# Kernel optimization log

Hardware: AMD Instinct MI355X
Metric: run time of the kernel (lower is better)

The kernel has to match this reference:

```python
import jax, jax.numpy as jnp
import numpy as np

B, N, IN_DIM, OUT = 4, 4096, 3, 40
NPTS = [1024, 256, 64, 16]   # base_points // sampling_ratio
K, FIRST_K = 8, 16
EPS = 1e-5

def gelu(t):
    return jax.nn.gelu(t, approximate=False)  # torch nn.GELU default (erf)

def pdist2(a, b):
    # a: (b,d,m), b: (b,d,n) -> squared pairwise distances (b,m,n)
    aa = jnp.sum(a * a, axis=1)[:, :, None]
    bb = jnp.sum(b * b, axis=1)[:, None, :]
    return aa + bb - 2.0 * jnp.einsum('bdm,bdn->bmn', a, b)

def knn_idx(a, b, k):
    # indices of k nearest points of b for each point of a
    return jax.lax.top_k(-pdist2(a, b), k)[1]

def gather_nbr(x, ind):
    # x: (b,d,n), ind: (b,m,k) -> (b,d,m,k)
    b, d, n = x.shape
    m, k = ind.shape[1], ind.shape[2]
    idx = jnp.broadcast_to(ind.reshape(b, 1, m * k), (b, d, m * k))
    return jnp.take_along_axis(x, idx, axis=2).reshape(b, d, m, k)

def bn(x):
    # BatchNorm (training-mode batch stats, gamma=1, beta=0 as at init)
    ax = (0,) + tuple(range(2, x.ndim))
    mu = jnp.mean(x, axis=ax, keepdims=True)
    var = jnp.mean((x - mu) ** 2, axis=ax, keepdims=True)
    return (x - mu) / jnp.sqrt(var + EPS)

def route(x, nbr):
    # (b,d,n),(b,n,k) -> (b,2d,n,k) : cat([neighbor - center, center])
    sel = gather_nbr(x, nbr)
    xc = x[:, :, :, None]
    return jnp.concatenate([sel - xc, jnp.broadcast_to(xc, sel.shape)], axis=1)

def edge_conv(x, l1, l2, sc, k, nbr=None):
    if nbr is None:
        nbr = knn_idx(x, x, k)  # dynamic graph in feature space
    h = jnp.max(jnp.einsum('of,bfnk->bonk', l1, route(x, nbr)), axis=-1)
    h = gelu(bn(h))
    h = jnp.max(jnp.einsum('of,bfnk->bonk', l2, route(h, nbr)), axis=-1)
    short = x if sc is None else jnp.einsum('of,bfn->bon', sc, x)
    return gelu(bn(short + h))

def fps(xyz, m):
    # farthest point sampling; xyz: (b,3,n) -> indices (b,m); start index 0
    pts = jnp.transpose(xyz, (0, 2, 1))  # (b,n,3)
    b, n, _ = pts.shape
    def body(carry, _):
        dmin, last = carry
        lp = jnp.take_along_axis(pts, last[:, None, None], axis=1)  # (b,1,3)
        d = jnp.sum((pts - lp) ** 2, axis=-1)
        dmin = jnp.minimum(dmin, d)
        nxt = jnp.argmax(dmin, axis=-1).astype(jnp.int32)
        return (dmin, nxt), last
    init = (jnp.full((b, n), jnp.inf, pts.dtype), jnp.zeros((b,), jnp.int32))
    _, inds = jax.lax.scan(body, init, None, length=m)
    return jnp.transpose(inds)  # (b,m)

def _forward(x, xyz, mlp_w, mlp_b, c0_l1, c0_l2, l1s, l2s, scs,
             head_w1, head_w2, head_b2):
    b = x.shape[0]
    nbr0 = knn_idx(xyz, xyz, FIRST_K)
    h = gelu(bn(jnp.einsum('oi,bin->bon', mlp_w, x) + mlp_b[None, :, None]))
    h = edge_conv(h, c0_l1, c0_l2, None, FIRST_K, nbr=nbr0)
    cur = xyz
    for i in range(4):
        m = NPTS[i]
        sind = fps(cur, m)
        sxyz = jnp.take_along_axis(
            cur, jnp.broadcast_to(sind[:, None, :], (b, cur.shape[1], m)), axis=2)
        nbr = knn_idx(sxyz, cur, K)
        cur = jnp.mean(gather_nbr(cur, nbr), axis=-1)      # sampled xyz = nbr mean
        h = jnp.max(gather_nbr(h, nbr), axis=-1)           # sampled feat = nbr max
        h = edge_conv(h, l1s[i], l2s[i], scs[i], K)
    g = jnp.mean(h, axis=-1)                               # global average pool
    g = gelu(bn(g @ head_w1.T))
    return g @ head_w2.T + head_b2[None, :]


def setup_inputs() -> dict:
    key = jax.random.key(0)
    ks = jax.random.split(key, 20)
    def w(k, o, i):
        return (jax.random.normal(k, (o, i), jnp.float32) / np.sqrt(i)).astype(jnp.float32)
    return {
        'x': jax.random.normal(ks[0], (B, IN_DIM, N), jnp.float32),
        'xyz': jax.random.normal(ks[1], (B, 3, N), jnp.float32),
        'mlp_w': w(ks[2], 64, IN_DIM), 'mlp_b': jnp.zeros((64,), jnp.float32),
        'c0_l1': w(ks[3], 64, 128), 'c0_l2': w(ks[4], 64, 128),
        's0_l1': w(ks[5], 64, 128), 's0_l2': w(ks[6], 64, 128),
        's1_l1': w(ks[7], 128, 128), 's1_l2': w(ks[8], 128, 256), 's1_sc': w(ks[9], 128, 64),
        's2_l1': w(ks[10], 256, 256), 's2_l2': w(ks[11], 256, 512), 's2_sc': w(ks[12], 256, 128),
        's3_l1': w(ks[13], 512, 512), 's3_l2': w(ks[14], 512, 1024), 's3_sc': w(ks[15], 512, 256),
        'head_w1': w(ks[16], 256, 512), 'head_w2': w(ks[17], OUT, 256),
        'head_b2': jnp.zeros((OUT,), jnp.float32),
    }


def reference(x, xyz, mlp_w, mlp_b, c0_l1, c0_l2, s0_l1, s0_l2,
              s1_l1, s1_l2, s1_sc, s2_l1, s2_l2, s2_sc, s3_l1, s3_l2, s3_sc,
              head_w1, head_w2, head_b2):
    return _forward(x, xyz, mlp_w, mlp_b, c0_l1, c0_l2,
                    (s0_l1, s1_l1, s2_l1, s3_l1),
                    (s0_l2, s1_l2, s2_l2, s3_l2),
                    (None, s1_sc, s2_sc, s3_sc),
                    head_w1, head_w2, head_b2)
```

## Files before the change

kernel.cpp:

```cpp
#include <hip/hip_runtime.h>
#include <math.h>

#define NCHUNK 32
typedef unsigned long long ull;

__device__ __forceinline__ float gelu_f(float v){
  return 0.5f*v*(1.0f+erff(v*0.70710678118654752440f));
}

__device__ __forceinline__ unsigned flipf(float d){
  unsigned u = __float_as_uint(d);
  return (u & 0x80000000u) ? ~u : (u | 0x80000000u);
}

template<int CTRL>
__device__ __forceinline__ ull dpp64(ull k){
  int lo = __builtin_amdgcn_update_dpp(0, (int)(unsigned)k,       CTRL, 0xF, 0xF, true);
  int hi = __builtin_amdgcn_update_dpp(0, (int)(unsigned)(k>>32), CTRL, 0xF, 0xF, true);
  return ((ull)(unsigned)hi<<32) | (unsigned)lo;
}
__device__ __forceinline__ ull rl64(ull k, int l){
  unsigned lo = (unsigned)__builtin_amdgcn_readlane((int)(unsigned)k, l);
  unsigned hi = (unsigned)__builtin_amdgcn_readlane((int)(unsigned)(k>>32), l);
  return ((ull)hi<<32) | lo;
}
__device__ __forceinline__ ull fmax64(ull a, ull b){
  return (ull)__double_as_longlong(fmax(__longlong_as_double((long long)a),
                                        __longlong_as_double((long long)b)));
}
__device__ __forceinline__ ull wave_fmax(ull k){
  k = fmax64(k, dpp64<0xB1>(k));
  k = fmax64(k, dpp64<0x4E>(k));
  k = fmax64(k, dpp64<0x141>(k));
  k = fmax64(k, dpp64<0x140>(k));
  ull a=rl64(k,0), b=rl64(k,16), c=rl64(k,32), d=rl64(k,48);
  return fmax64(fmax64(a,b), fmax64(c,d));
}
template<int CTRL>
__device__ __forceinline__ double dmin_dpp(double k){
  ull o = dpp64<CTRL>((ull)__double_as_longlong(k));
  return fmin(k, __longlong_as_double((long long)o));
}
__device__ __forceinline__ double wave_dmin(double k){
  k = dmin_dpp<0xB1>(k);
  k = dmin_dpp<0x4E>(k);
  k = dmin_dpp<0x141>(k);
  k = dmin_dpp<0x140>(k);
  ull kb = (ull)__double_as_longlong(k);
  double a = __longlong_as_double((long long)rl64(kb,0));
  double b = __longlong_as_double((long long)rl64(kb,16));
  double c = __longlong_as_double((long long)rl64(kb,32));
  double d = __longlong_as_double((long long)rl64(kb,48));
  return fmin(fmin(a,b), fmin(c,d));
}


template<int K, int T>
__device__ __forceinline__ void knn_body(
    const float* __restrict__ cand, int n,
    const float* __restrict__ qsrc, const int* __restrict__ qidx, int m,
    int* __restrict__ nbr, float* __restrict__ outc,
    int b, int qblk, int qoff, char* smem)
{
  float4* tile = (float4*)smem;
  constexpr int NWV = T/64;
  int wv = threadIdx.x >> 6, lane = threadIdx.x & 63;
  int q = qblk*NWV + wv + qoff;
  const float* cb = cand + (size_t)b*3*n;
  int qi = qidx ? qidx[(size_t)b*m + q] : q;
  const float* qb = qsrc + (size_t)b*3*n;
  float qx = qb[qi], qy = qb[n+qi], qz = qb[2*n+qi];
  float aa = (qx*qx + qy*qy) + qz*qz;

  double a[K];
  #pragma unroll
  for (int k=0;k<K;k++) a[k] = 1e300;

  for (int base=0; base<n; base+=1024){
    int cnt = min(1024, n-base);
    for (int j=threadIdx.x; j<cnt; j+=T){
      float x=cb[base+j], y=cb[n+base+j], z=cb[2*n+base+j];
      tile[j] = make_float4(x,y,z,(x*x+y*y)+z*z);
    }
    __syncthreads();
    int steps = cnt >> 6;
    double jd = (double)(base + lane);
    for (int i=0;i<steps;i++){
      int j = lane + (i<<6);
      float4 c = tile[j];
      float d = aa + c.w - 2.0f*((qx*c.x+qy*c.y)+qz*c.z);
      double key = (double)flipf(d) * 4096.0 + jd;
      if (key < a[K-1]){
        #pragma unroll
        for (int k=K-1;k>=1;k--)
          a[k] = fmin(fmax(a[k-1], key), a[k]);
        a[0] = fmin(a[0], key);
      }
      jd += 64.0;
    }
    __syncthreads();
  }

  double head = a[0];
  int res[K];
  #pragma unroll
  for (int r=0; r<K; r++){
    double mk = wave_dmin(head);
    res[r] = (int)((ull)mk & 4095u);
    if (head == mk){
      #pragma unroll
      for (int i2=0;i2<K-1;i2++) a[i2]=a[i2+1];
      a[K-1] = 1e300;
      head = a[0];
    }
  }
  if (lane == 0){
    int* o = nbr + ((size_t)b*m + q)*K;
    #pragma unroll
    for (int r=0;r<K;r++) o[r] = res[r];
  }
  if (outc != nullptr && lane < 3){
    const float* cd = cb + (size_t)lane*n;
    float s=0;
    #pragma unroll
    for (int k=0;k<K;k++) s += cd[res[k]];
    outc[((size_t)b*3 + lane)*m + q] = s * (1.0f/K);
  }
}

template<int NP, int T, int M>
__device__ __forceinline__ void fps_mw_seg(const float* __restrict__ cur, int n,
                                           int* __restrict__ sind, float* __restrict__ gdmin,
                                           int b, int M0, int M1, char* smem)
{
  constexpr int NW = T/64;
  int tid = threadIdx.x;
  int wv = tid>>6;
  const float* cb = cur + (size_t)b*3*n;
  float4* lp = (float4*)smem;
  ull* wred = (ull*)(smem + sizeof(float4)*NP*T);
  float* gd = gdmin + (size_t)b*n;
  float px[NP], py[NP], pz[NP], dmin[NP];
  unsigned nj[NP];
  #pragma unroll
  for (int s=0;s<NP;s++){
    int j = tid + s*T;
    px[s]=cb[j]; py[s]=cb[n+j]; pz[s]=cb[2*n+j];
    dmin[s] = (M0==0) ? 1e30f : gd[j];
    nj[s] = (unsigned)(~j);
    lp[j] = make_float4(px[s],py[s],pz[s],0.f);
  }
  __syncthreads();
  int ci = (M0==0) ? 0 : sind[(size_t)b*M + (M0-1)];
  float4 w0 = lp[ci];
  float X = w0.x, Y = w0.y, Z = w0.z;
  if (M0==0 && tid==0) sind[(size_t)b*M] = 0;
  __builtin_amdgcn_s_setprio(3);
  int p = 0;
  int s0 = (M0==0) ? 1 : M0;
  for (int step=s0; step<M1; step++){
    ull key[NP];
    #pragma unroll
    for (int s=0;s<NP;s++){
      float dx=px[s]-X, dy=py[s]-Y, dz=pz[s]-Z;
      float d = (dx*dx + dy*dy) + dz*dz;
      float nd = fminf(dmin[s], d);
      dmin[s] = nd;
      key[s] = ((ull)__float_as_uint(nd)<<32) | nj[s];
    }
    #pragma unroll
    for (int w=NP; w>1; w>>=1)
      #pragma unroll
      for (int i=0;i<NP;i++) if (i < (w>>1))
        key[i] = fmax64(key[i], key[i+(w>>1)]);
    ull wk = wave_fmax(key[0]);
    if ((tid&63)==0) wred[p*NW + wv] = wk;
    __syncthreads();
    const ulonglong2* wp2 = (const ulonglong2*)(wred + p*NW);
    ulonglong2 m0 = wp2[0], m1 = wp2[1], m2 = wp2[2], m3 = wp2[3];
    ull gk = fmax64(fmax64(fmax64(m0.x,m0.y), fmax64(m1.x,m1.y)),
                    fmax64(fmax64(m2.x,m2.y), fmax64(m3.x,m3.y)));
    int gi = (int)(~(unsigned)gk);
    if (tid==0) sind[(size_t)b*M + step] = gi;
    float4 wp = lp[gi];
    X=wp.x; Y=wp.y; Z=wp.z;
    p ^= 1;
  }
  __builtin_amdgcn_s_setprio(0);
  #pragma unroll
  for (int s=0;s<NP;s++) gd[tid + s*T] = dmin[s];
}

template<int NP, int M>
__device__ __forceinline__ void fps_sw_body(const float* __restrict__ cur, int n,
                                            int* __restrict__ sind, int b, char* smem)
{
  int lane = threadIdx.x;
  const float* cb = cur + (size_t)b*3*n;
  float4* lp = (float4*)smem;
  float px[NP], py[NP], pz[NP], dmin[NP];
  unsigned nj[NP];
  #pragma unroll
  for (int s=0;s<NP;s++){
    int j = lane + s*64;
    px[s]=cb[j]; py[s]=cb[n+j]; pz[s]=cb[2*n+j]; dmin[s]=1e30f;
    nj[s] = (unsigned)(~j);
    lp[j] = make_float4(px[s],py[s],pz[s],0.f);
  }
  float X = lp[0].x, Y = lp[0].y, Z = lp[0].z;
  if (lane==0) sind[(size_t)b*M] = 0;
  __builtin_amdgcn_s_setprio(3);
  for (int step=1; step<M; step++){
    ull key[NP];
    #pragma unroll
    for (int s=0;s<NP;s++){
      float dx=px[s]-X, dy=py[s]-Y, dz=pz[s]-Z;
      float d = (dx*dx + dy*dy) + dz*dz;
      float nd = fminf(dmin[s], d);
      dmin[s] = nd;
      key[s] = ((ull)__float_as_uint(nd)<<32) | nj[s];
    }
    #pragma unroll
    for (int w=NP; w>1; w>>=1)
      #pragma unroll
      for (int i=0;i<NP;i++) if (i < (w>>1))
        key[i] = fmax64(key[i], key[i+(w>>1)]);
    ull gk = wave_fmax(key[0]);
    int gi = (int)(~(unsigned)gk);
    if (lane==0) sind[(size_t)b*M + step] = gi;
    float4 wp = lp[gi];
    X=wp.x; Y=wp.y; Z=wp.z;
  }
  __builtin_amdgcn_s_setprio(0);
}

template<bool DUAL, bool BN>
__device__ __forceinline__ void gemm_body(
    const float* __restrict__ A, const float* __restrict__ B,
    float* __restrict__ out0, float* __restrict__ out1,
    int M, int N, int Kd, int lda, int ldb, int ldo, int boff,
    long sA, long sB, long sO, const float* __restrict__ part, float invR,
    int bxi, int byi, int bzi, char* smem)
{
  A += (size_t)bzi * sA; B += (size_t)bzi * sB;
  float* o0 = out0 + (size_t)bzi * sO;
  float* o1 = DUAL ? (out1 + (size_t)bzi * sO) : nullptr;
  int rowBase = byi*64, colBase = bxi*64;
  float (*As)[64]  = (float(*)[64])smem;
  float (*Bs0)[64] = (float(*)[64])(smem + 4096);
  float (*Bs1)[64] = (float(*)[64])(smem + 8192);
  float* mu_s = (float*)(smem + 12288);
  float* var_s = mu_s + 512;
  int tid = threadIdx.x;
  if (BN){
    for (int oo=tid; oo<Kd; oo+=blockDim.x){
      float s=0, q=0;
      #pragma unroll 4
      for (int c=0;c<NCHUNK;c++){
        s += part[(size_t)c*1024 + oo];
        q += part[(size_t)(NCHUNK+c)*1024 + oo];
      }
      float mu = s*invR;
      mu_s[oo] = mu;
      var_s[oo] = q*invR - mu*mu;
    }
    __syncthreads();
  }
  int ty = tid>>4, tx = tid&15;
  float acc0[4][4] = {}, acc1[4][4] = {};
  int lr = tid>>2, lk = (tid&3)*4;
  for (int k0=0; k0<Kd; k0+=16) {
    float4 va = make_float4(0,0,0,0);
    int r = rowBase + lr;
    if (r < M) va = *(const float4*)(A + (size_t)r*lda + k0 + lk);
    if (BN){
      int c = k0 + lk;
      va.x = gelu_f((va.x - mu_s[c+0]) / sqrtf(var_s[c+0] + 1e-5f));
      va.y = gelu_f((va.y - mu_s[c+1]) / sqrtf(var_s[c+1] + 1e-5f));
      va.z = gelu_f((va.z - mu_s[c+2]) / sqrtf(var_s[c+2] + 1e-5f));
      va.w = gelu_f((va.w - mu_s[c+3]) / sqrtf(var_s[c+3] + 1e-5f));
    }
    As[lk+0][lr]=va.x; As[lk+1][lr]=va.y; As[lk+2][lr]=va.z; As[lk+3][lr]=va.w;
    float4 vb = make_float4(0,0,0,0), vb2 = make_float4(0,0,0,0);
    int c2 = colBase + lr;
    if (c2 < N) {
      vb = *(const float4*)(B + (size_t)c2*ldb + k0 + lk);
      if (DUAL) vb2 = *(const float4*)(B + (size_t)c2*ldb + boff + k0 + lk);
    }
    Bs0[lk+0][lr]=vb.x; Bs0[lk+1][lr]=vb.y; Bs0[lk+2][lr]=vb.z; Bs0[lk+3][lr]=vb.w;
    if (DUAL) {
      Bs1[lk+0][lr]=vb2.x-vb.x; Bs1[lk+1][lr]=vb2.y-vb.y;
      Bs1[lk+2][lr]=vb2.z-vb.z; Bs1[lk+3][lr]=vb2.w-vb.w;
    }
    __syncthreads();
    #pragma unroll
    for (int kk=0;kk<16;kk++){
      float4 a  = *(const float4*)&As[kk][ty*4];
      float4 b0 = *(const float4*)&Bs0[kk][tx*4];
      float av[4]={a.x,a.y,a.z,a.w};
      float b0v[4]={b0.x,b0.y,b0.z,b0.w};
      #pragma unroll
      for (int i=0;i<4;i++)
        #pragma unroll
        for (int j=0;j<4;j++) acc0[i][j] = fmaf(av[i], b0v[j], acc0[i][j]);
      if (DUAL) {
        float4 b1 = *(const float4*)&Bs1[kk][tx*4];
        float b1v[4]={b1.x,b1.y,b1.z,b1.w};
        #pragma unroll
        for (int i=0;i<4;i++)
          #pragma unroll
          for (int j=0;j<4;j++) acc1[i][j] = fmaf(av[i], b1v[j], acc1[i][j]);
      }
    }
    __syncthreads();
  }
  #pragma unroll
  for (int i=0;i<4;i++){
    int r = rowBase + ty*4 + i;
    if (r < M) {
      #pragma unroll
      for (int j=0;j<4;j++){
        int c = colBase + tx*4 + j;
        if (c < N) {
          o0[(size_t)r*ldo + c] = acc0[i][j];
          if (DUAL) o1[(size_t)r*ldo + c] = acc1[i][j];
        }
      }
    }
  }
}

template<bool DUAL, bool BN>
__device__ __forceinline__ void gemm_body_g(
    const float* __restrict__ A, const float* __restrict__ B,
    float* __restrict__ out0, float* __restrict__ out1,
    int M, int N, int Kd, int lda, int ldb, int ldo, int boff,
    const float* __restrict__ part, float invR,
    int bxi, int byi, char* smem)
{
  int rowBase = byi*64, colBase = bxi*64;
  float (*As)[64]  = (float(*)[64])smem;
  float (*Bs0)[64] = (float(*)[64])(smem + 4096);
  float (*Bs1)[64] = (float(*)[64])(smem + 8192);
  float* mu_s = (float*)(smem + 12288);
  float* var_s = mu_s + 512;
  int tid = threadIdx.x;
  bool act = tid < 256;
  if (BN){
    for (int oo=tid; oo<Kd; oo+=blockDim.x){
      float s=0, q=0;
      #pragma unroll 4
      for (int c=0;c<NCHUNK;c++){
        s += part[(size_t)c*1024 + oo];
        q += part[(size_t)(NCHUNK+c)*1024 + oo];
      }
      float mu = s*invR;
      mu_s[oo] = mu;
      var_s[oo] = q*invR - mu*mu;
    }
    __syncthreads();
  }
  int ty = tid>>4, tx = tid&15;
  float acc0[4][4] = {}, acc1[4][4] = {};
  int lr = tid>>2, lk = (tid&3)*4;
  for (int k0=0; k0<Kd; k0+=16) {
    if (act){
      float4 va = make_float4(0,0,0,0);
      int r = rowBase + lr;
      if (r < M) va = *(const float4*)(A + (size_t)r*lda + k0 + lk);
      if (BN){
        int c = k0 + lk;
        va.x = gelu_f((va.x - mu_s[c+0]) / sqrtf(var_s[c+0] + 1e-5f));
        va.y = gelu_f((va.y - mu_s[c+1]) / sqrtf(var_s[c+1] + 1e-5f));
        va.z = gelu_f((va.z - mu_s[c+2]) / sqrtf(var_s[c+2] + 1e-5f));
        va.w = gelu_f((va.w - mu_s[c+3]) / sqrtf(var_s[c+3] + 1e-5f));
      }
      As[lk+0][lr]=va.x; As[lk+1][lr]=va.y; As[lk+2][lr]=va.z; As[lk+3][lr]=va.w;
      float4 vb = make_float4(0,0,0,0), vb2 = make_float4(0,0,0,0);
      int c2 = colBase + lr;
      if (c2 < N) {
        vb = *(const float4*)(B + (size_t)c2*ldb + k0 + lk);
        if (DUAL) vb2 = *(const float4*)(B + (size_t)c2*ldb + boff + k0 + lk);
      }
      Bs0[lk+0][lr]=vb.x; Bs0[lk+1][lr]=vb.y; Bs0[lk+2][lr]=vb.z; Bs0[lk+3][lr]=vb.w;
      if (DUAL) {
        Bs1[lk+0][lr]=vb2.x-vb.x; Bs1[lk+1][lr]=vb2.y-vb.y;
        Bs1[lk+2][lr]=vb2.z-vb.z; Bs1[lk+3][lr]=vb2.w-vb.w;
      }
    }
    __syncthreads();
    if (act){
      #pragma unroll
      for (int kk=0;kk<16;kk++){
        float4 a  = *(const float4*)&As[kk][ty*4];
        float4 b0 = *(const float4*)&Bs0[kk][tx*4];
        float av[4]={a.x,a.y,a.z,a.w};
        float b0v[4]={b0.x,b0.y,b0.z,b0.w};
        #pragma unroll
        for (int i=0;i<4;i++)
          #pragma unroll
          for (int j=0;j<4;j++) acc0[i][j] = fmaf(av[i], b0v[j], acc0[i][j]);
        if (DUAL) {
          float4 b1 = *(const float4*)&Bs1[kk][tx*4];
          float b1v[4]={b1.x,b1.y,b1.z,b1.w};
          #pragma unroll
          for (int i=0;i<4;i++)
            #pragma unroll
            for (int j=0;j<4;j++) acc1[i][j] = fmaf(av[i], b1v[j], acc1[i][j]);
        }
      }
    }
    __syncthreads();
  }
  if (act){
    #pragma unroll
    for (int i=0;i<4;i++){
      int r = rowBase + ty*4 + i;
      if (r < M) {
        #pragma unroll
        for (int j=0;j<4;j++){
          int c = colBase + tx*4 + j;
          if (c < N) {
            out0[(size_t)r*ldo + c] = acc0[i][j];
            if (DUAL) out1[(size_t)r*ldo + c] = acc1[i][j];
          }
        }
      }
    }
  }
}

__device__ __forceinline__ void gather_elem(
    const float* __restrict__ P, const int* __restrict__ nbr,
    const float* __restrict__ addA, const float* __restrict__ addB,
    float* __restrict__ out, int n_out, int n_src, int O, int K, int total, int e)
{
  if (e >= total) return;
  int o = e % O; int r = e / O;
  int b = r / n_out; int i = r % n_out;
  const int* nb = nbr + ((size_t)b*n_out + i)*K;
  float mx = -1e38f;
  for (int k=0;k<K;k++){
    int j = nb[k];
    float v = P[((size_t)b*n_src + j)*O + o];
    mx = fmaxf(mx, v);
  }
  float res = mx;
  if (addA) res += addA[e];
  if (addB) res = addB[e] + res;
  out[e] = res;
}

__device__ __forceinline__ void gatherbn_body(
    const float* __restrict__ P, const int* __restrict__ nbr,
    const float* __restrict__ part, float invR,
    float* __restrict__ out, float* __restrict__ aa,
    int n_out, int n_src, int O, int K, int blk, char* smem)
{
  float* mu_s = (float*)smem; float* var_s = mu_s + 256; float* sv = var_s + 256;
  int tid = threadIdx.x;
  for (int oo=tid; oo<O; oo+=256){
    float s=0, q=0;
    #pragma unroll 4
    for (int c=0;c<NCHUNK;c++){
      s += part[(size_t)c*1024 + oo];
      q += part[(size_t)(NCHUNK+c)*1024 + oo];
    }
    float mu = s*invR;
    mu_s[oo] = mu;
    var_s[oo] = q*invR - mu*mu;
  }
  __syncthreads();
  int e = blk*256 + tid;
  int o = e % O; int r = e / O;
  int b = r / n_out; int i = r % n_out;
  const int* nb = nbr + ((size_t)b*n_out + i)*K;
  float mu = mu_s[o], sd = sqrtf(var_s[o] + 1e-5f);
  float mx = -1e38f;
  for (int k=0;k<K;k++){
    int j = nb[k];
    float p = P[((size_t)b*n_src + j)*O + o];
    float v = gelu_f((p - mu)/sd);
    mx = fmaxf(mx, v);
  }
  out[e] = mx;
  sv[tid] = mx*mx;
  __syncthreads();
  for (int st=O>>1; st>0; st>>=1){
    if (o < st) sv[tid] += sv[tid+st];
    __syncthreads();
  }
  if (o == 0) aa[r] = sv[tid];
}


#define FPS_SMEM 65664

__global__ __launch_bounds__(512,2) void mega1(
    const float* __restrict__ xyz, const float* __restrict__ x,
    const float* __restrict__ mlpw, const float* __restrict__ mlpb,
    int* __restrict__ sind0, float* __restrict__ gdmin,
    int* __restrict__ nbr0, float* __restrict__ hA, int M0, int M1)
{
  __shared__ __align__(16) char SMEM[FPS_SMEM];
  int bid = blockIdx.x;
  if (bid < 4){
    fps_mw_seg<8,512,1024>(xyz, 4096, sind0, gdmin, bid, M0, M1, SMEM);
  } else if (bid < 4+2048){
    int kb = bid - 4;
    knn_body<16,512>(xyz, 4096, xyz, nullptr, 4096, nbr0, nullptr, kb>>9, kb&511, 0, SMEM);
  } else {
    int e = (bid - 2052)*512 + threadIdx.x;
    if (e < 4*4096*64){
      int o = e & 63; int r = e >> 6;
      int b = r / 4096; int i = r % 4096;
      const float* xb = x + (size_t)b*3*4096;
      hA[e] = ((mlpw[o*3+0]*xb[i] + mlpw[o*3+1]*xb[4096+i]) + mlpw[o*3+2]*xb[2*4096+i]) + mlpb[o];
    }
  }
}

__global__ __launch_bounds__(512,2) void fps_bngelu(
    const float* fcur, int* sind, float* gdmin, int M0, int M1,
    float* __restrict__ xx, const float* __restrict__ part, float invR, int O, int total)
{
  __shared__ __align__(16) char SMEM[FPS_SMEM];
  if (blockIdx.x < 4){
    fps_mw_seg<8,512,1024>(fcur, 4096, sind, gdmin, blockIdx.x, M0, M1, SMEM);
    return;
  }
  float* mu_s = (float*)SMEM; float* var_s = mu_s + 512;
  for (int oo=threadIdx.x; oo<O; oo+=512){
    float s=0, q=0;
    #pragma unroll 4
    for (int c=0;c<NCHUNK;c++){
      s += part[(size_t)c*1024 + oo];
      q += part[(size_t)(NCHUNK+c)*1024 + oo];
    }
    float mu = s*invR;
    mu_s[oo] = mu;
    var_s[oo] = q*invR - mu*mu;
  }
  __syncthreads();
  int e = (blockIdx.x-4)*512 + threadIdx.x;
  if (e >= total) return;
  int o = e % O;
  float v = (xx[e]-mu_s[o]) / sqrtf(var_s[o] + 1e-5f);
  xx[e] = gelu_f(v);
}

template<bool DUAL, bool BN>
__global__ __launch_bounds__(512,2) void fps0_gemm(
    const float* fcur, int* sind, float* gdmin, int M0, int M1,
    const float* A, const float* B, float* out0, float* out1,
    int Mg, int Ng, int Kd, int lda, int ldb, int ldo, int boff,
    const float* part, float invR, int nbx)
{
  __shared__ __align__(16) char SMEM[FPS_SMEM];
  if (blockIdx.x < 4){
    fps_mw_seg<8,512,1024>(fcur, 4096, sind, gdmin, blockIdx.x, M0, M1, SMEM);
    return;
  }
  int l = blockIdx.x - 4;
  gemm_body_g<DUAL,BN>(A,B,out0,out1,Mg,Ng,Kd,lda,ldb,ldo,boff,part,invR, l%nbx, l/nbx, SMEM);
}

__global__ __launch_bounds__(512,2) void fps0_gather_knn(
    const float* fcur, int* sind, float* gdmin, int M0, int M1,
    const float* cand, int n, const float* qsrc, const int* qidx, int m,
    int* nbrOut, float* outc, int KNB,
    const float* P, const int* nbr, const float* addA, const float* addB,
    float* out, int n_out, int n_src, int O, int K, int total)
{
  __shared__ __align__(16) char SMEM[FPS_SMEM];
  if (blockIdx.x < 4){
    fps_mw_seg<8,512,1024>(fcur, 4096, sind, gdmin, blockIdx.x, M0, M1, SMEM);
    return;
  }
  int l = blockIdx.x - 4;
  if (l < KNB){
    knn_body<8,512>(cand, n, qsrc, qidx, m, nbrOut, outc, l>>6, l&63, 0, SMEM);
    return;
  }
  int e = (l-KNB)*512 + threadIdx.x;
  gather_elem(P, nbr, addA, addB, out, n_out, n_src, O, K, total, e);
}

__global__ __launch_bounds__(512,2) void fps0_gather(
    const float* fcur, int* sind, float* gdmin, int M0, int M1,
    const float* P, const int* nbr, const float* addA, const float* addB,
    float* out, int n_out, int n_src, int O, int K, int total)
{
  __shared__ __align__(16) char SMEM[FPS_SMEM];
  if (blockIdx.x < 4){
    fps_mw_seg<8,512,1024>(fcur, 4096, sind, gdmin, blockIdx.x, M0, M1, SMEM);
    return;
  }
  int e = (blockIdx.x-4)*512 + threadIdx.x;
  gather_elem(P, nbr, addA, addB, out, n_out, n_src, O, K, total, e);
}

__global__ __launch_bounds__(512,2) void fps0_stats(
    const float* fcur, int* sind, float* gdmin, int M0, int M1,
    const float* __restrict__ x, int R, int O, float* __restrict__ part)
{
  __shared__ __align__(16) char SMEM[FPS_SMEM];
  if (blockIdx.x < 4){
    fps_mw_seg<8,512,1024>(fcur, 4096, sind, gdmin, blockIdx.x, M0, M1, SMEM);
    return;
  }
  int o = threadIdx.x;
  if (o >= O) return;
  int chunk = blockIdx.x - 4;
  int per = (R + NCHUNK - 1)/NCHUNK;
  int r0 = chunk*per, r1 = min(r0+per, R);
  float s=0, q=0;
  for (int r=r0; r<r1; r++){ float v = x[(size_t)r*O + o]; s+=v; q+=v*v; }
  part[(size_t)chunk*1024 + o] = s;
  part[(size_t)(NCHUNK+chunk)*1024 + o] = q;
}

__global__ __launch_bounds__(256) void knn_wave8(
    const float* cand, int n, const float* qsrc, const int* qidx, int m, int qoff,
    int* nbr, float* outc)
{
  __shared__ __align__(16) char SMEM[16384];
  knn_body<8,256>(cand, n, qsrc, qidx, m, nbr, outc, blockIdx.y, blockIdx.x, qoff, SMEM);
}

template<int NP, int M>
__global__ __launch_bounds__(256) void fps_gatherbn(
    const float* fcur, int fn, int* sind,
    const float* P, const int* nbr, const float* part, float invR,
    float* out, float* aa, int n_out, int n_src, int O, int K)
{
  __shared__ __align__(16) char SMEM[(NP*64*16 > 16384) ? NP*64*16 : 16384];
  if (blockIdx.x < 4){
    if (threadIdx.x < 64) fps_sw_body<NP,M>(fcur, fn, sind, blockIdx.x, SMEM);
    return;
  }
  gatherbn_body(P, nbr, part, invR, out, aa, n_out, n_src, O, K, blockIdx.x-4, SMEM);
}

template<int NP, int M, bool DUAL, bool BN>
__global__ __launch_bounds__(256) void fps_gemm(
    const float* fcur, int fn, int* sind,
    const float* A, const float* B, float* out0, float* out1,
    int Mg, int Ng, int Kd, int lda, int ldb, int ldo, int boff,
    const float* part, float invR, int nbx, int nby)
{
  __shared__ __align__(16) char SMEM[(NP*64*16 > 16896) ? NP*64*16 : 16896];
  if (blockIdx.x < 4){
    if (threadIdx.x < 64) fps_sw_body<NP,M>(fcur, fn, sind, blockIdx.x, SMEM);
    return;
  }
  int l = blockIdx.x - 4;
  int bx = l % nbx, by = (l/nbx) % nby, bz = l/(nbx*nby);
  gemm_body<DUAL,BN>(A,B,out0,out1,Mg,Ng,Kd,lda,ldb,ldo,boff,0,0,0,part,invR,bx,by,bz,SMEM);
}

__global__ __launch_bounds__(256) void knn_gather(
    const float* cand, int n, const float* qsrc, const int* qidx, int m,
    int* nbrOut, float* outc, int KNB,
    const float* P, const int* nbr, const float* addA, const float* addB,
    float* out, int n_out, int n_src, int O, int K, int total)
{
  __shared__ __align__(16) char SMEM[16384];
  if (blockIdx.x < KNB){
    int qpb = m/4;
    knn_body<8,256>(cand, n, qsrc, qidx, m, nbrOut, outc, blockIdx.x/qpb, blockIdx.x%qpb, 0, SMEM);
    return;
  }
  gather_elem(P, nbr, addA, addB, out, n_out, n_src, O, K, total, (blockIdx.x-KNB)*256 + threadIdx.x);
}

__global__ __launch_bounds__(256) void knn_gemm(
    const float* cand, int n, const float* qsrc, const int* qidx, int m,
    int* nbrOut, float* outc, int KNB,
    const float* A, const float* B, float* out0,
    int Mg, int Ng, int Kd, int lda, int ldb, int ldo,
    long sA, long sB, long sO, int nbx, int nby)
{
  __shared__ __align__(16) char SMEM[16896];
  if (blockIdx.x < KNB){
    int qpb = m/4;
    knn_body<8,256>(cand, n, qsrc, qidx, m, nbrOut, outc, blockIdx.x/qpb, blockIdx.x%qpb, 0, SMEM);
    return;
  }
  int l = blockIdx.x - KNB;
  int bx = l % nbx, by = (l/nbx) % nby, bz = l/(nbx*nby);
  gemm_body<false,false>(A,B,out0,nullptr,Mg,Ng,Kd,lda,ldb,ldo,0,sA,sB,sO,nullptr,0.f,bx,by,bz,SMEM);
}

__global__ __launch_bounds__(256) void gram_gemm(
    const float* Ag, float* outg, int Mg, int Kg, long sAg, long sOg,
    int ngx, int ngy, int NG,
    const float* A2, const float* B2, float* o20, float* o21,
    int M2, int N2, int K2, int boff2, int nb2x)
{
  __shared__ __align__(16) char SMEM[16896];
  int l = blockIdx.x;
  if (l < NG){
    int bx = l % ngx, by = (l/ngx) % ngy, bz = l/(ngx*ngy);
    gemm_body<false,false>(Ag,Ag,outg,nullptr,Mg,Mg,Kg,Kg,Kg,Mg,0,sAg,sAg,sOg,nullptr,0.f,bx,by,bz,SMEM);
    return;
  }
  l -= NG;
  gemm_body<true,false>(A2,B2,o20,o21,M2,N2,K2,K2,2*K2,N2,boff2,0,0,0,nullptr,0.f, l%nb2x, l/nb2x, 0, SMEM);
}

template<bool DUAL, bool BN>
__global__ __launch_bounds__(256) void gemm_nt(
    const float* A, const float* B, float* out0, float* out1,
    int M, int N, int Kd, int lda, int ldb, int ldo, int boff,
    long sA, long sB, long sO, const float* part, float invR)
{
  __shared__ __align__(16) char SMEM[16896];
  gemm_body<DUAL,BN>(A,B,out0,out1,M,N,Kd,lda,ldb,ldo,boff,sA,sB,sO,part,invR,
                     blockIdx.x, blockIdx.y, blockIdx.z, SMEM);
}

__global__ __launch_bounds__(256) void gemm2sc(
    const float* A2, const float* B2, float* o20, float* o21, int R, int O2, int O1v,
    const float* part, float invR,
    const float* Asc, const float* Bsc, float* osc, int Cin,
    int nbx, int nby)
{
  __shared__ __align__(16) char SMEM[16896];
  int l = blockIdx.x;
  int half = nbx*nby;
  if (l < half){
    gemm_body<true,true>(A2,B2,o20,o21,R,O2,O1v,O1v,2*O1v,O2,O1v,0,0,0,part,invR, l%nbx, l/nbx, 0, SMEM);
  } else {
    l -= half;
    gemm_body<false,false>(Asc,Bsc,osc,nullptr,R,O2,Cin,Cin,Cin,O2,0,0,0,0,nullptr,0.f, l%nbx, l/nbx, 0, SMEM);
  }
}

__global__ __launch_bounds__(256) void gathermax_kernel(
    const float* P, const int* nbr, const float* addA, const float* addB,
    float* out, int n_out, int n_src, int O, int K, int total)
{
  gather_elem(P, nbr, addA, addB, out, n_out, n_src, O, K, total, blockIdx.x*256 + threadIdx.x);
}

__global__ __launch_bounds__(256) void gatherbn_kernel(
    const float* P, const int* nbr, const float* part, float invR,
    float* out, float* aa, int n_out, int n_src, int O, int K)
{
  __shared__ __align__(16) char SMEM[3072];
  gatherbn_body(P, nbr, part, invR, out, aa, n_out, n_src, O, K, blockIdx.x, SMEM);
}

template<int K>
__global__ __launch_bounds__(256) void topk_wave(
    const float* __restrict__ G, const float* __restrict__ aa, int m,
    int* __restrict__ nbr)
{
  __shared__ float abs_s[1024];
  int b = blockIdx.y;
  int wv = threadIdx.x >> 6, lane = threadIdx.x & 63;
  int q = blockIdx.x*4 + wv;
  const float* ab = aa + (size_t)b*m;
  for (int j=threadIdx.x; j<m; j+=256) abs_s[j] = ab[j];
  __syncthreads();
  float aq = ab[q];
  const float* Gq = G + ((size_t)b*m + q)*m;

  double a[K];
  #pragma unroll
  for (int k=0;k<K;k++) a[k] = 1e300;

  int steps = (m+63)>>6;
  double jd = (double)lane;
  for (int i=0;i<steps;i++){
    int j = lane + (i<<6);
    double key = 1e300;
    if (j < m){
      float g = Gq[j];
      float d = aq + abs_s[j] - 2.0f*g;
      key = (double)flipf(d) * 4096.0 + jd;
    }
    if (key < a[K-1]){
      #pragma unroll
      for (int k=K-1;k>=1;k--)
        a[k] = fmin(fmax(a[k-1], key), a[k]);
      a[0] = fmin(a[0], key);
    }
    jd += 64.0;
  }
  double head = a[0];
  int res[K];
  #pragma unroll
  for (int r=0; r<K; r++){
    double mk = wave_dmin(head);
    res[r] = (int)((ull)mk & 4095u);
    if (head == mk){
      #pragma unroll
      for (int i2=0;i2<K-1;i2++) a[i2]=a[i2+1];
      a[K-1] = 1e300;
      head = a[0];
    }
  }
  if (lane == 0){
    int* o = nbr + ((size_t)b*m + q)*K;
    #pragma unroll
    for (int r=0;r<K;r++) o[r] = res[r];
  }
}

__global__ void stats_part_kernel(const float* __restrict__ x, int R, int O,
                                  float* __restrict__ part)
{
  int o = threadIdx.x;
  int chunk = blockIdx.x;
  int per = (R + NCHUNK - 1)/NCHUNK;
  int r0 = chunk*per, r1 = min(r0+per, R);
  float s=0, q=0;
  for (int r=r0; r<r1; r++){ float v = x[(size_t)r*O + o]; s+=v; q+=v*v; }
  part[(size_t)chunk*1024 + o] = s;
  part[(size_t)(NCHUNK+chunk)*1024 + o] = q;
}

__global__ __launch_bounds__(1024) void head_kernel(const float* __restrict__ h,
    const float* __restrict__ part, float invR,
    const float* __restrict__ w1, const float* __restrict__ w2,
    const float* __restrict__ b2, float* __restrict__ out)
{
  __shared__ __align__(16) float mu_s[512], var_s[512];
  __shared__ __align__(16) float g[4*512];
  __shared__ __align__(16) float t[4*256];
  int tid = threadIdx.x;
  for (int oo=tid; oo<512; oo+=1024){
    float s=0, q=0;
    #pragma unroll 4
    for (int c=0;c<NCHUNK;c++){
      s += part[(size_t)c*1024 + oo];
      q += part[(size_t)(NCHUNK+c)*1024 + oo];
    }
    float mu = s*invR;
    mu_s[oo] = mu;
    var_s[oo] = q*invR - mu*mu;
  }
  __syncthreads();
  for (int e=tid; e<2048; e+=1024){
    int b=e>>9, c=e&511;
    float mu = mu_s[c], sd = sqrtf(var_s[c] + 1e-5f);
    float s=0;
    for (int p=0;p<16;p++){
      float v = h[((size_t)(b*16+p))*512 + c];
      s += gelu_f((v-mu)/sd);
    }
    g[e] = s * (1.0f/16.0f);
  }
  __syncthreads();
  {
    int b = tid>>8, j = tid&255;
    const float4* gr = (const float4*)(g + b*512);
    const float4* wr = (const float4*)(w1 + (size_t)j*512);
    float s=0;
    for (int c=0;c<128;c++){
      float4 a=gr[c], w=wr[c];
      s = fmaf(a.x,w.x, fmaf(a.y,w.y, fmaf(a.z,w.z, fmaf(a.w,w.w, s))));
    }
    t[tid] = s;
  }
  __syncthreads();
  if (tid < 256){
    float v0=t[tid], v1=t[256+tid], v2=t[512+tid], v3=t[768+tid];
    float mu = ((v0+v1)+v2+v3)*0.25f;
    float d0=v0-mu, d1=v1-mu, d2=v2-mu, d3=v3-mu;
    float var = ((d0*d0+d1*d1)+d2*d2+d3*d3)*0.25f;
    float sq = sqrtf(var + 1e-5f);
    t[tid]     = gelu_f(d0/sq);
    t[256+tid] = gelu_f(d1/sq);
    t[512+tid] = gelu_f(d2/sq);
    t[768+tid] = gelu_f(d3/sq);
  }
  __syncthreads();
  if (tid < 160){
    int b = tid/40, o = tid%40;
    const float* tr = t + b*256; const float* wr = w2 + (size_t)o*256;
    float s=0;
    for (int j=0;j<256;j++) s = fmaf(tr[j], wr[j], s);
    out[tid] = s + b2[o];
  }
}

extern "C" void kernel_launch(void* const* d_in, const int* in_sizes, int n_in,
                              void* d_out, int out_size, void* d_ws, size_t ws_size,
                              hipStream_t stream)
{
  const float* x    = (const float*)d_in[0];
  const float* xyz  = (const float*)d_in[1];
  const float* mlpw = (const float*)d_in[2];
  const float* mlpb = (const float*)d_in[3];
  const float* c0l1 = (const float*)d_in[4];
  const float* c0l2 = (const float*)d_in[5];
  const float* L1[4] = {(const float*)d_in[6], (const float*)d_in[8],
                        (const float*)d_in[11], (const float*)d_in[14]};
  const float* L2[4] = {(const float*)d_in[7], (const float*)d_in[9],
                        (const float*)d_in[12], (const float*)d_in[15]};
  const float* SC[4] = {nullptr, (const float*)d_in[10],
                        (const float*)d_in[13], (const float*)d_in[16]};
  const float* hw1 = (const float*)d_in[17];
  const float* hw2 = (const float*)d_in[18];
  const float* hb2 = (const float*)d_in[19];
  float* out = (float*)d_out;

  float* ws = (float*)d_ws;
  const size_t MF = 1024*1024;
  float* D    = ws;
  float* hA   = ws + 4*MF;
  float* hX   = ws + 5*MF;
  float* hP   = ws + 6*MF;
  float* hCT  = ws + 7*MF;
  float* hSH  = ws + 8*MF;
  float* hH1  = ws + 9*MF;
  float* hOUT = ws + 10*MF;
  float* aux  = ws + 11*MF;
  int*   nbr0  = (int*)aux;                 aux += 262144;
  int*   nbrS0 = (int*)aux;                 aux += 32768;
  int*   nbrS1 = (int*)aux;                 aux += 8192;
  int*   nbrS2 = (int*)aux;                 aux += 2048;
  int*   nbrS3 = (int*)aux;                 aux += 512;
  int*   nbrF  = (int*)aux;                 aux += 32768;
  int*   sind0 = (int*)aux;                 aux += 4096;
  int*   sind1 = (int*)aux;                 aux += 1024;
  int*   sind2 = (int*)aux;                 aux += 256;
  int*   sind3 = (int*)aux;                 aux += 64;
  float* aa    = aux;                       aux += 4096;
  float* cur1  = aux;                       aux += 12288;
  float* cur2  = aux;                       aux += 3072;
  float* cur3  = aux;                       aux += 768;
  float* part  = aux;                       aux += 65536;
  float* gdmin = aux;                       aux += 16384;

  int tot0 = 4*4096*64;

  mega1<<<4100, 512, 0, stream>>>(xyz, x, mlpw, mlpb, sind0, gdmin, nbr0, hA, 0, 260);
  stats_part_kernel<<<NCHUNK, 64, 0, stream>>>(hA, 16384, 64, part);
  fps_bngelu<<<4+2048, 512, 0, stream>>>(xyz, sind0, gdmin, 260, 390, hA, part, 1.0f/16384.0f, 64, tot0);
  fps0_gemm<true,false><<<4+256, 512, 0, stream>>>(xyz, sind0, gdmin, 390, 517,
      hA, c0l1, hP, hCT, 16384, 64, 64, 64, 128, 64, 64, nullptr, 0.f, 1);
  fps0_gather_knn<<<4+256+2048, 512, 0, stream>>>(xyz, sind0, gdmin, 517, 644,
      xyz, 4096, xyz, sind0, 1024, nbrS0, cur1, 256,
      hP, nbr0, hCT, nullptr, hH1, 4096, 4096, 64, 16, 1048576);
  stats_part_kernel<<<NCHUNK, 64, 0, stream>>>(hH1, 16384, 64, part);
  fps0_gemm<true,true><<<4+256, 512, 0, stream>>>(xyz, sind0, gdmin, 644, 771,
      hH1, c0l2, hP, hCT, 16384, 64, 64, 64, 128, 64, 64, part, 1.0f/16384.0f, 1);
  fps0_gather<<<4+2048, 512, 0, stream>>>(xyz, sind0, gdmin, 771, 898,
      hP, nbr0, hCT, hA, hOUT, 4096, 4096, 64, 16, 1048576);
  fps0_stats<<<4+NCHUNK, 512, 0, stream>>>(xyz, sind0, gdmin, 898, 1024,
      hOUT, 16384, 64, part);

  knn_wave8<<<dim3(128,4),256,0,stream>>>(xyz, 4096, xyz, sind0, 1024, 512, nbrS0, cur1);

  fps_gatherbn<16,256><<<4+1024,256,0,stream>>>(cur1, 1024, sind1,
      hOUT, nbrS0, part, 1.0f/16384.0f, hX, aa, 1024, 4096, 64, 8);
  knn_gemm<<<256+1024,256,0,stream>>>(cur1, 1024, cur1, sind1, 256, nbrS1, cur2, 256,
      hX, hX, D, 1024, 1024, 64, 64, 64, 1024,
      (long)1024*64, (long)1024*64, (long)1024*1024, 16, 16);
  topk_wave<8><<<dim3(256,4),256,0,stream>>>(D, aa, 1024, nbrF);
  fps_gemm<4,64,true,false><<<4+64,256,0,stream>>>(cur2, 256, sind2,
      hX, L1[0], hP, hCT, 4096, 64, 64, 64, 128, 64, 64, nullptr, 0.f, 1, 64);
  knn_gather<<<64+1024,256,0,stream>>>(cur2, 256, cur2, sind2, 64, nbrS2, cur3, 64,
      hP, nbrF, hCT, nullptr, hH1, 1024, 1024, 64, 8, 262144);
  stats_part_kernel<<<NCHUNK, 64, 0, stream>>>(hH1, 4096, 64, part);
  fps_gemm<1,16,true,true><<<4+64,256,0,stream>>>(cur3, 64, sind3,
      hH1, L2[0], hP, hCT, 4096, 64, 64, 64, 128, 64, 64, part, 1.0f/4096.0f, 1, 64);
  knn_gather<<<16+1024,256,0,stream>>>(cur3, 64, cur3, sind3, 16, nbrS3, nullptr, 16,
      hP, nbrF, hCT, hX, hA, 1024, 1024, 64, 8, 262144);
  stats_part_kernel<<<NCHUNK, 64, 0, stream>>>(hA, 4096, 64, part);

  const int   mArr[3]   = {256, 64, 16};
  const int   nsrcArr[3]= {1024, 256, 64};
  const int   CinArr[3] = {64, 128, 256};
  const int   OArr[3]   = {128, 256, 512};
  const int*  nbrSs[3]  = {nbrS1, nbrS2, nbrS3};
  float* hcur = hA;
  float invRprev = 1.0f/4096.0f;
  for (int s=0;s<3;s++){
    int m = mArr[s], nsrc = nsrcArr[s], Cin = CinArr[s], O1 = OArr[s], O2 = OArr[s];
    int R = 4*m;
    int th = R*Cin;
    gatherbn_kernel<<<th/256,256,0,stream>>>(hcur, nbrSs[s], part, invRprev,
                                             hX, aa, m, nsrc, Cin, 8);
    int ngx = (m+63)/64, ngy = (m+63)/64;
    int NG = ngx*ngy*4;
    int nb1x = (O1+63)/64, nb1y = (R+63)/64;
    gram_gemm<<<NG + nb1x*nb1y, 256, 0, stream>>>(
        hX, D, m, Cin, (long)m*Cin, (long)m*m, ngx, ngy, NG,
        hX, L1[s+1], hP, hCT, R, O1, Cin, Cin, nb1x);
    topk_wave<8><<<dim3(m/4,4),256,0,stream>>>(D, aa, m, nbrF);
    int t1 = R*O1;
    gathermax_kernel<<<(t1+255)/256,256,0,stream>>>(hP, nbrF, hCT, nullptr, hH1, m, m, O1, 8, t1);
    stats_part_kernel<<<NCHUNK, O1, 0, stream>>>(hH1, R, O1, part);
    int nbx = (O2+63)/64, nby = (R+63)/64;
    gemm2sc<<<2*nbx*nby,256,0,stream>>>(hH1, L2[s+1], hP, hCT, R, O2, O1, part, 1.0f/R,
                                        hX, SC[s+1], hSH, Cin, nbx, nby);
    int t2 = R*O2;
    float* outbuf = (s&1) ? hA : hOUT;
    gathermax_kernel<<<(t2+255)/256,256,0,stream>>>(hP, nbrF, hCT, hSH, outbuf, m, m, O2, 8, t2);
    stats_part_kernel<<<NCHUNK, O2, 0, stream>>>(outbuf, R, O2, part);
    hcur = outbuf;
    invRprev = 1.0f/R;
  }

  head_kernel<<<1,1024,0,stream>>>(hcur, part, 1.0f/64.0f, hw1, hw2, hb2, out);
}
```

Before: 1.558 ms.

## Split stage-1 FPS across three kernels and re-pair side tasks to overlap serial work

The 256-step FPS over 1024 points now runs in three resumable segments, carrying min-distances through a global buffer. Each segment rides alongside the gatherbn, gram GEMM and top-k kernels. The later FPS and KNN launches are re-paired with different GEMM and gather work, and the first loop iteration's gatherbn is folded into a KNN launch. The aim is to hide the serial, single-wave FPS chains behind parallel work and cut launches, at the cost of extra global save/restore traffic and more complex dependencies between kernels.

```diff
diff --git a/kernel.cpp b/kernel.cpp
--- a/kernel.cpp
+++ b/kernel.cpp
@@ -125,6 +125,62 @@
     #pragma unroll
     for (int k=0;k<K;k++) s += cd[res[k]];
     outc[((size_t)b*3 + lane)*m + q] = s * (1.0f/K);
+  }
+}
+
+template<int K>
+__device__ __forceinline__ void topk_body(
+    const float* __restrict__ G, const float* __restrict__ aa, int m,
+    int* __restrict__ nbr, int b, int qblk, char* smem)
+{
+  float* abs_s = (float*)smem;
+  int wv = threadIdx.x >> 6, lane = threadIdx.x & 63;
+  int q = qblk*4 + wv;
+  const float* ab = aa + (size_t)b*m;
+  for (int j=threadIdx.x; j<m; j+=256) abs_s[j] = ab[j];
+  __syncthreads();
+  float aq = ab[q];
+  const float* Gq = G + ((size_t)b*m + q)*m;
+
+  double a[K];
+  #pragma unroll
+  for (int k=0;k<K;k++) a[k] = 1e300;
+
+  int steps = (m+63)>>6;
+  double jd = (double)lane;
+  for (int i=0;i<steps;i++){
+    int j = lane + (i<<6);
+    double key = 1e300;
+    if (j < m){
+      float g = Gq[j];
+      float d = aq + abs_s[j] - 2.0f*g;
+      key = (double)flipf(d) * 4096.0 + jd;
+    }
+    if (key < a[K-1]){
+      #pragma unroll
+      for (int k=K-1;k>=1;k--)
+        a[k] = fmin(fmax(a[k-1], key), a[k]);
+      a[0] = fmin(a[0], key);
+    }
+    jd += 64.0;
+  }
+  double head = a[0];
+  int res[K];
+  #pragma unroll
+  for (int r=0; r<K; r++){
+    double mk = wave_dmin(head);
+    res[r] = (int)((ull)mk & 4095u);
+    if (head == mk){
+      #pragma unroll
+      for (int i2=0;i2<K-1;i2++) a[i2]=a[i2+1];
+      a[K-1] = 1e300;
+      head = a[0];
+    }
+  }
+  if (lane == 0){
+    int* o = nbr + ((size_t)b*m + q)*K;
+    #pragma unroll
+    for (int r=0;r<K;r++) o[r] = res[r];
   }
 }
 
@@ -232,6 +288,57 @@
     X=wp.x; Y=wp.y; Z=wp.z;
   }
   __builtin_amdgcn_s_setprio(0);
+}
+
+template<int NP, int M>
+__device__ __forceinline__ void fps_sw_seg(const float* __restrict__ cur, int n,
+                                           int* __restrict__ sind, float* __restrict__ gdmin,
+                                           int b, int M0, int M1, char* smem)
+{
+  int lane = threadIdx.x;
+  const float* cb = cur + (size_t)b*3*n;
+  float4* lp = (float4*)smem;
+  float* gd = gdmin + (size_t)b*n;
+  float px[NP], py[NP], pz[NP], dmin[NP];
+  unsigned nj[NP];
+  #pragma unroll
+  for (int s=0;s<NP;s++){
+    int j = lane + s*64;
+    px[s]=cb[j]; py[s]=cb[n+j]; pz[s]=cb[2*n+j];
+    dmin[s] = (M0==0) ? 1e30f : gd[j];
+    nj[s] = (unsigned)(~j);
+    lp[j] = make_float4(px[s],py[s],pz[s],0.f);
+  }
+  int ci = (M0==0) ? 0 : sind[(size_t)b*M + (M0-1)];
+  float4 w0 = lp[ci];
+  float X = w0.x, Y = w0.y, Z = w0.z;
+  if (M0==0 && lane==0) sind[(size_t)b*M] = 0;
+  __builtin_amdgcn_s_setprio(3);
+  int s0 = (M0==0) ? 1 : M0;
+  for (int step=s0; step<M1; step++){
+    ull key[NP];
+    #pragma unroll
+    for (int s=0;s<NP;s++){
+      float dx=px[s]-X, dy=py[s]-Y, dz=pz[s]-Z;
+      float d = (dx*dx + dy*dy) + dz*dz;
+      float nd = fminf(dmin[s], d);
+      dmin[s] = nd;
+      key[s] = ((ull)__float_as_uint(nd)<<32) | nj[s];
+    }
+    #pragma unroll
+    for (int w=NP; w>1; w>>=1)
+      #pragma unroll
+      for (int i=0;i<NP;i++) if (i < (w>>1))
+        key[i] = fmax64(key[i], key[i+(w>>1)]);
+    ull gk = wave_fmax(key[0]);
+    int gi = (int)(~(unsigned)gk);
+    if (lane==0) sind[(size_t)b*M + step] = gi;
+    float4 wp = lp[gi];
+    X=wp.x; Y=wp.y; Z=wp.z;
+  }
+  __builtin_amdgcn_s_setprio(0);
+  #pragma unroll
+  for (int s=0;s<NP;s++) gd[lane + s*64] = dmin[s];
 }
 
 template<bool DUAL, bool BN>
@@ -628,58 +735,68 @@
   knn_body<8,256>(cand, n, qsrc, qidx, m, nbr, outc, blockIdx.y, blockIdx.x, qoff, SMEM);
 }
 
-template<int NP, int M>
-__global__ __launch_bounds__(256) void fps_gatherbn(
-    const float* fcur, int fn, int* sind,
+__global__ __launch_bounds__(256) void fps1_gatherbn(
+    const float* fcur, int* sind, float* gdmin, int M0, int M1,
     const float* P, const int* nbr, const float* part, float invR,
     float* out, float* aa, int n_out, int n_src, int O, int K)
 {
-  __shared__ __align__(16) char SMEM[(NP*64*16 > 16384) ? NP*64*16 : 16384];
+  __shared__ __align__(16) char SMEM[16384];
+  if (blockIdx.x < 4){
+    if (threadIdx.x < 64) fps_sw_seg<16,256>(fcur, 1024, sind, gdmin, blockIdx.x, M0, M1, SMEM);
+    return;
+  }
+  gatherbn_body(P, nbr, part, invR, out, aa, n_out, n_src, O, K, blockIdx.x-4, SMEM);
+}
+
+__global__ __launch_bounds__(256) void fps1_gram(
+    const float* fcur, int* sind, float* gdmin, int M0, int M1,
+    const float* Ag, float* outg, int Mg, int Kg, long sAg, long sOg, int ngx, int ngy)
+{
+  __shared__ __align__(16) char SMEM[16896];
+  if (blockIdx.x < 4){
+    if (threadIdx.x < 64) fps_sw_seg<16,256>(fcur, 1024, sind, gdmin, blockIdx.x, M0, M1, SMEM);
+    return;
+  }
+  int l = blockIdx.x - 4;
+  int bx = l % ngx, by = (l/ngx) % ngy, bz = l/(ngx*ngy);
+  gemm_body<false,false>(Ag,Ag,outg,nullptr,Mg,Mg,Kg,Kg,Kg,Mg,0,sAg,sAg,sOg,nullptr,0.f,bx,by,bz,SMEM);
+}
+
+__global__ __launch_bounds__(256) void fps1_topk(
+    const float* fcur, int* sind, float* gdmin, int M0, int M1,
+    const float* G, const float* aa, int m, int* nbr)
+{
+  __shared__ __align__(16) char SMEM[16384];
+  if (blockIdx.x < 4){
+    if (threadIdx.x < 64) fps_sw_seg<16,256>(fcur, 1024, sind, gdmin, blockIdx.x, M0, M1, SMEM);
+    return;
+  }
+  int l = blockIdx.x - 4;
+  int qpb = m/4;
+  topk_body<8>(G, aa, m, nbr, l/qpb, l%qpb, SMEM);
+}
+
+template<int NP, int M>
+__global__ __launch_bounds__(256) void fps_gather(
+    const float* fcur, int fn, int* sind,
+    const float* P, const int* nbr, const float* addA, const float* addB,
+    float* out, int n_out, int n_src, int O, int K, int total)
+{
+  __shared__ __align__(16) char SMEM[(NP*64*16 > 4096) ? NP*64*16 : 4096];
   if (blockIdx.x < 4){
     if (threadIdx.x < 64) fps_sw_body<NP,M>(fcur, fn, sind, blockIdx.x, SMEM);
     return;
   }
-  gatherbn_body(P, nbr, part, invR, out, aa, n_out, n_src, O, K, blockIdx.x-4, SMEM);
-}
-
-template<int NP, int M, bool DUAL, bool BN>
-__global__ __launch_bounds__(256) void fps_gemm(
-    const float* fcur, int fn, int* sind,
-    const float* A, const float* B, float* out0, float* out1,
-    int Mg, int Ng, int Kd, int lda, int ldb, int ldo, int boff,
-    const float* part, float invR, int nbx, int nby)
-{
-  __shared__ __align__(16) char SMEM[(NP*64*16 > 16896) ? NP*64*16 : 16896];
-  if (blockIdx.x < 4){
-    if (threadIdx.x < 64) fps_sw_body<NP,M>(fcur, fn, sind, blockIdx.x, SMEM);
-    return;
-  }
-  int l = blockIdx.x - 4;
-  int bx = l % nbx, by = (l/nbx) % nby, bz = l/(nbx*nby);
-  gemm_body<DUAL,BN>(A,B,out0,out1,Mg,Ng,Kd,lda,ldb,ldo,boff,0,0,0,part,invR,bx,by,bz,SMEM);
-}
-
-__global__ __launch_bounds__(256) void knn_gather(
+  gather_elem(P, nbr, addA, addB, out, n_out, n_src, O, K, total, (blockIdx.x-4)*256 + threadIdx.x);
+}
+
+template<bool DUAL, bool BN>
+__global__ __launch_bounds__(256) void knn_gemm2(
     const float* cand, int n, const float* qsrc, const int* qidx, int m,
     int* nbrOut, float* outc, int KNB,
-    const float* P, const int* nbr, const float* addA, const float* addB,
-    float* out, int n_out, int n_src, int O, int K, int total)
-{
-  __shared__ __align__(16) char SMEM[16384];
-  if (blockIdx.x < KNB){
-    int qpb = m/4;
-    knn_body<8,256>(cand, n, qsrc, qidx, m, nbrOut, outc, blockIdx.x/qpb, blockIdx.x%qpb, 0, SMEM);
-    return;
-  }
-  gather_elem(P, nbr, addA, addB, out, n_out, n_src, O, K, total, (blockIdx.x-KNB)*256 + threadIdx.x);
-}
-
-__global__ __launch_bounds__(256) void knn_gemm(
-    const float* cand, int n, const float* qsrc, const int* qidx, int m,
-    int* nbrOut, float* outc, int KNB,
-    const float* A, const float* B, float* out0,
-    int Mg, int Ng, int Kd, int lda, int ldb, int ldo,
-    long sA, long sB, long sO, int nbx, int nby)
+    const float* A, const float* B, float* out0, float* out1,
+    int Mg, int Ng, int Kd, int boff,
+    const float* part, float invR, int nbx)
 {
   __shared__ __align__(16) char SMEM[16896];
   if (blockIdx.x < KNB){
@@ -688,8 +805,22 @@
     return;
   }
   int l = blockIdx.x - KNB;
-  int bx = l % nbx, by = (l/nbx) % nby, bz = l/(nbx*nby);
-  gemm_body<false,false>(A,B,out0,nullptr,Mg,Ng,Kd,lda,ldb,ldo,0,sA,sB,sO,nullptr,0.f,bx,by,bz,SMEM);
+  gemm_body<DUAL,BN>(A,B,out0,out1,Mg,Ng,Kd,Kd,DUAL?2*Kd:Kd,Ng,boff,0,0,0,part,invR, l%nbx, l/nbx, 0, SMEM);
+}
+
+__global__ __launch_bounds__(256) void knn_gatherbn(
+    const float* cand, int n, const float* qsrc, const int* qidx, int m,
+    int* nbrOut, int KNB,
+    const float* P, const int* nbr, const float* part, float invR,
+    float* out, float* aa, int n_out, int n_src, int O, int K)
+{
+  __shared__ __align__(16) char SMEM[16384];
+  if (blockIdx.x < KNB){
+    int qpb = m/4;
+    knn_body<8,256>(cand, n, qsrc, qidx, m, nbrOut, nullptr, blockIdx.x/qpb, blockIdx.x%qpb, 0, SMEM);
+    return;
+  }
+  gatherbn_body(P, nbr, part, invR, out, aa, n_out, n_src, O, K, blockIdx.x-KNB, SMEM);
 }
 
 __global__ __launch_bounds__(256) void gram_gemm(
@@ -707,17 +838,6 @@
   }
   l -= NG;
   gemm_body<true,false>(A2,B2,o20,o21,M2,N2,K2,K2,2*K2,N2,boff2,0,0,0,nullptr,0.f, l%nb2x, l/nb2x, 0, SMEM);
-}
-
-template<bool DUAL, bool BN>
-__global__ __launch_bounds__(256) void gemm_nt(
-    const float* A, const float* B, float* out0, float* out1,
-    int M, int N, int Kd, int lda, int ldb, int ldo, int boff,
-    long sA, long sB, long sO, const float* part, float invR)
-{
-  __shared__ __align__(16) char SMEM[16896];
-  gemm_body<DUAL,BN>(A,B,out0,out1,M,N,Kd,lda,ldb,ldo,boff,sA,sB,sO,part,invR,
-                     blockIdx.x, blockIdx.y, blockIdx.z, SMEM);
 }
 
 __global__ __launch_bounds__(256) void gemm2sc(
@@ -757,56 +877,8 @@
     const float* __restrict__ G, const float* __restrict__ aa, int m,
     int* __restrict__ nbr)
 {
-  __shared__ float abs_s[1024];
-  int b = blockIdx.y;
-  int wv = threadIdx.x >> 6, lane = threadIdx.x & 63;
-  int q = blockIdx.x*4 + wv;
-  const float* ab = aa + (size_t)b*m;
-  for (int j=threadIdx.x; j<m; j+=256) abs_s[j] = ab[j];
-  __syncthreads();
-  float aq = ab[q];
-  const float* Gq = G + ((size_t)b*m + q)*m;
-
-  double a[K];
-  #pragma unroll
-  for (int k=0;k<K;k++) a[k] = 1e300;
-
-  int steps = (m+63)>>6;
-  double jd = (double)lane;
-  for (int i=0;i<steps;i++){
-    int j = lane + (i<<6);
-    double key = 1e300;
-    if (j < m){
-      float g = Gq[j];
-      float d = aq + abs_s[j] - 2.0f*g;
-      key = (double)flipf(d) * 4096.0 + jd;
-    }
-    if (key < a[K-1]){
-      #pragma unroll
-      for (int k=K-1;k>=1;k--)
-        a[k] = fmin(fmax(a[k-1], key), a[k]);
-      a[0] = fmin(a[0], key);
-    }
-    jd += 64.0;
-  }
-  double head = a[0];
-  int res[K];
-  #pragma unroll
-  for (int r=0; r<K; r++){
-    double mk = wave_dmin(head);
-    res[r] = (int)((ull)mk & 4095u);
-    if (head == mk){
-      #pragma unroll
-      for (int i2=0;i2<K-1;i2++) a[i2]=a[i2+1];
-      a[K-1] = 1e300;
-      head = a[0];
-    }
-  }
-  if (lane == 0){
-    int* o = nbr + ((size_t)b*m + q)*K;
-    #pragma unroll
-    for (int r=0;r<K;r++) o[r] = res[r];
-  }
+  __shared__ __align__(16) char SMEM[4096];
+  topk_body<K>(G, aa, m, nbr, blockIdx.y, blockIdx.x, SMEM);
 }
 
 __global__ void stats_part_kernel(const float* __restrict__ x, int R, int O,
@@ -956,22 +1028,27 @@
 
   knn_wave8<<<dim3(128,4),256,0,stream>>>(xyz, 4096, xyz, sind0, 1024, 512, nbrS0, cur1);
 
-  fps_gatherbn<16,256><<<4+1024,256,0,stream>>>(cur1, 1024, sind1,
+  fps1_gatherbn<<<4+1024,256,0,stream>>>(cur1, sind1, gdmin, 0, 86,
       hOUT, nbrS0, part, 1.0f/16384.0f, hX, aa, 1024, 4096, 64, 8);
-  knn_gemm<<<256+1024,256,0,stream>>>(cur1, 1024, cur1, sind1, 256, nbrS1, cur2, 256,
-      hX, hX, D, 1024, 1024, 64, 64, 64, 1024,
-      (long)1024*64, (long)1024*64, (long)1024*1024, 16, 16);
-  topk_wave<8><<<dim3(256,4),256,0,stream>>>(D, aa, 1024, nbrF);
-  fps_gemm<4,64,true,false><<<4+64,256,0,stream>>>(cur2, 256, sind2,
-      hX, L1[0], hP, hCT, 4096, 64, 64, 64, 128, 64, 64, nullptr, 0.f, 1, 64);
-  knn_gather<<<64+1024,256,0,stream>>>(cur2, 256, cur2, sind2, 64, nbrS2, cur3, 64,
+  fps1_gram<<<4+1024,256,0,stream>>>(cur1, sind1, gdmin, 86, 171,
+      hX, D, 1024, 64, (long)1024*64, (long)1024*1024, 16, 16);
+  fps1_topk<<<4+1024,256,0,stream>>>(cur1, sind1, gdmin, 171, 256,
+      D, aa, 1024, nbrF);
+  knn_gemm2<true,false><<<256+64,256,0,stream>>>(cur1, 1024, cur1, sind1, 256,
+      nbrS1, cur2, 256,
+      hX, L1[0], hP, hCT, 4096, 64, 64, 64, nullptr, 0.f, 1);
+  fps_gather<4,64><<<4+1024,256,0,stream>>>(cur2, 256, sind2,
       hP, nbrF, hCT, nullptr, hH1, 1024, 1024, 64, 8, 262144);
   stats_part_kernel<<<NCHUNK, 64, 0, stream>>>(hH1, 4096, 64, part);
-  fps_gemm<1,16,true,true><<<4+64,256,0,stream>>>(cur3, 64, sind3,
-      hH1, L2[0], hP, hCT, 4096, 64, 64, 64, 128, 64, 64, part, 1.0f/4096.0f, 1, 64);
-  knn_gather<<<16+1024,256,0,stream>>>(cur3, 64, cur3, sind3, 16, nbrS3, nullptr, 16,
+  knn_gemm2<true,true><<<64+64,256,0,stream>>>(cur2, 256, cur2, sind2, 64,
+      nbrS2, cur3, 64,
+      hH1, L2[0], hP, hCT, 4096, 64, 64, 64, part, 1.0f/4096.0f, 1);
+  fps_gather<1,16><<<4+1024,256,0,stream>>>(cur3, 64, sind3,
       hP, nbrF, hCT, hX, hA, 1024, 1024, 64, 8, 262144);
   stats_part_kernel<<<NCHUNK, 64, 0, stream>>>(hA, 4096, 64, part);
+  knn_gatherbn<<<16+256,256,0,stream>>>(cur3, 64, cur3, sind3, 16,
+      nbrS3, 16,
+      hA, nbrS1, part, 1.0f/4096.0f, hX, aa, 256, 1024, 64, 8);
 
   const int   mArr[3]   = {256, 64, 16};
   const int   nsrcArr[3]= {1024, 256, 64};
@@ -984,8 +1061,10 @@
     int m = mArr[s], nsrc = nsrcArr[s], Cin = CinArr[s], O1 = OArr[s], O2 = OArr[s];
     int R = 4*m;
     int th = R*Cin;
-    gatherbn_kernel<<<th/256,256,0,stream>>>(hcur, nbrSs[s], part, invRprev,
-                                             hX, aa, m, nsrc, Cin, 8);
+    if (s > 0){
+      gatherbn_kernel<<<th/256,256,0,stream>>>(hcur, nbrSs[s], part, invRprev,
+                                               hX, aa, m, nsrc, Cin, 8);
+    }
     int ngx = (m+63)/64, ngy = (m+63)/64;
     int NG = ngx*ngy*4;
     int nb1x = (O1+63)/64, nb1y = (R+63)/64;
```

Measured after the change: 1.553 ms. About the same (-0.3%).
